# Optimization experiments

Hardware: AMD Instinct MI355X
Metric: run time of the kernel (lower is better)

Reference implementation:

```python
import jax, jax.numpy as jnp
import numpy as np

N_NODES = 500_000
N_EDGES = 8_000_000
N_GRAPHS = 1000


def _mlp(x, w1, b1, w2, b2):
    # Linear -> SELU -> Linear (torch Sequential equivalent)
    return jax.nn.selu(x @ w1 + b1) @ w2 + b2


def setup_inputs() -> dict:
    key = jax.random.key(0)
    ks = jax.random.split(key, 25)
    p = lambda i, shape: jax.random.normal(ks[i], shape, jnp.float32) * 0.1
    return {
        "nodes": jax.random.normal(ks[0], (N_NODES, 1), jnp.float32),
        "edges": jax.random.normal(ks[1], (N_EDGES, 1), jnp.float32),
        "senders": jax.random.randint(ks[2], (N_EDGES,), 0, N_NODES),
        "receivers": jax.random.randint(ks[3], (N_EDGES,), 0, N_NODES),
        "graph_ids": jnp.sort(jax.random.randint(ks[4], (N_NODES,), 0, N_GRAPHS)),
        "num_graphs": N_GRAPHS,
        # permutate_nodes: 2 -> 10 -> 10
        "pn_w1": p(5, (2, 10)), "pn_b1": p(6, (10,)), "pn_w2": p(7, (10, 10)), "pn_b2": p(8, (10,)),
        # update_edges: 11 -> 5 -> 1
        "ue_w1": p(9, (11, 5)), "ue_b1": p(10, (5,)), "ue_w2": p(11, (5, 1)), "ue_b2": p(12, (1,)),
        # permutate_edges: 1 -> 5 -> 10
        "pe_w1": p(13, (1, 5)), "pe_b1": p(14, (5,)), "pe_w2": p(15, (5, 10)), "pe_b2": p(16, (10,)),
        # update_nodes: 11 -> 5 -> 1
        "un_w1": p(17, (11, 5)), "un_b1": p(18, (5,)), "un_w2": p(19, (5, 1)), "un_b2": p(20, (1,)),
        # predict: 11 -> 10 -> 10
        "pr_w1": p(21, (11, 10)), "pr_b1": p(22, (10,)), "pr_w2": p(23, (10, 10)), "pr_b2": p(24, (10,)),
    }


def reference(nodes, edges, pn_w1, pn_b1, pn_w2, pn_b2,
              ue_w1, ue_b1, ue_w2, ue_b2,
              pe_w1, pe_b1, pe_w2, pe_b2,
              un_w1, un_b1, un_w2, un_b2,
              pr_w1, pr_b1, pr_w2, pr_b2,
              senders, receivers, graph_ids, num_graphs):
    # gather node feats to edges: [recv || send] -> (E, 2)
    collected = jnp.concatenate([nodes[receivers], nodes[senders]], axis=-1)
    h1_nodes = _mlp(collected, pn_w1, pn_b1, pn_w2, pn_b2)  # (E, 10)
    h1_edges = edges  # (E, 1)
    for _ in range(3):
        h1_edges = _mlp(jnp.concatenate([h1_edges, h1_nodes], axis=-1),
                        ue_w1, ue_b1, ue_w2, ue_b2)  # (E, 1)
    # edges -> nodes aggregation (sum over receiver)
    edges_of_nodes = jax.ops.segment_sum(h1_edges, receivers, num_segments=nodes.shape[0])  # (N, 1)
    h2_edges = _mlp(edges_of_nodes, pe_w1, pe_b1, pe_w2, pe_b2)  # (N, 10)
    h2_nodes = nodes  # (N, 1)
    for _ in range(3):
        h2_nodes = _mlp(jnp.concatenate([h2_nodes, h2_edges], axis=-1),
                        un_w1, un_b1, un_w2, un_b2)  # (N, 1)
    # nodes -> globals aggregation (sum per graph)
    g = jax.ops.segment_sum(jnp.concatenate([h2_nodes, h2_edges], axis=-1),
                            graph_ids, num_segments=num_graphs)  # (G, 11)
    out = _mlp(g, pr_w1, pr_b1, pr_w2, pr_b2)  # (G, 10)
    return jax.nn.softmax(out, axis=-1)
```

## Files before the change

kernel.cpp:

```cpp
#include <hip/hip_runtime.h>
#include <hip/hip_fp16.h>
#include <math.h>

#define N_NODES_C  500000
#define N_EDGES_C  8000000
#define N_GRAPHS_C 1000
#define NGROUPS_C  (N_EDGES_C / 4)

#define BSHIFT  11
#define BWIDTH  2048
#define NBKT    245

#define P2_TPB  512
#define EPB2    8192
#define GPB2    (EPB2 / 4)
#define NPB2    ((NGROUPS_C + GPB2 - 1) / GPB2)
#define SROW2   992
#define RITER2  (GPB2 / P2_TPB)

#define GRAPH_ACC_OFF 0
#define PARTIALS_OFF  11008
#define FW_OFF        33024
#define ZERO_HEAD     33024

#define STARTS2_OFF   33280
#define PAIRS64_OFF   (STARTS2_OFF + 246 * SROW2)
#define WS2_WORDS_NEEDED (PAIRS64_OFF + NPB2 * EPB2 * 2)

#define OLD_NODE_ACC_OFF 33536
#define OLD_ZERO_WORDS   (OLD_NODE_ACC_OFF + N_NODES_C)

#define LOG2E_F 1.4426950408889634f


__device__ __forceinline__ float selu2(float xl) {
    const float C1 = 0.7282901039f;
    const float C2 = 1.7580993408473766f;
    float e = __builtin_amdgcn_exp2f(xl);
    float neg = fmaf(C2, e, -C2);
    return xl > 0.0f ? C1 * xl : neg;
}

__device__ __forceinline__ float selu_f(float x) {
    const float scale = 1.0507009873554805f;
    const float sa    = 1.0507009873554805f * 1.6732632423543772f;
    float neg = sa * (__expf(x) - 1.0f);
    return x > 0.0f ? scale * x : neg;
}

__device__ __forceinline__ void atomAddF(float* p, float v) {
    __hip_atomic_fetch_add(p, v, __ATOMIC_RELAXED, __HIP_MEMORY_SCOPE_AGENT);
}

__device__ __forceinline__ void fuse_weights(
        int t,
        const float* __restrict__ pn_w1, const float* __restrict__ pn_b1,
        const float* __restrict__ pn_w2, const float* __restrict__ pn_b2,
        const float* __restrict__ ue_w1, const float* __restrict__ ue_b1,
        const float* __restrict__ ue_w2, const float* __restrict__ ue_b2,
        const float* __restrict__ pe_w1, const float* __restrict__ pe_b1,
        const float* __restrict__ pe_w2, const float* __restrict__ pe_b2,
        const float* __restrict__ un_w1, const float* __restrict__ un_b1,
        const float* __restrict__ un_w2, const float* __restrict__ un_b2,
        float* __restrict__ fw) {
    const float L = LOG2E_F;
    if (t < 20) fw[0 + t] = pn_w1[t] * L;
    if (t < 10) fw[20 + t] = pn_b1[t] * L;
    if (t < 50) {
        int j = t / 5, k = t % 5;
        float s = 0.0f;
        for (int m = 0; m < 10; ++m) s += pn_w2[j * 10 + m] * ue_w1[(1 + m) * 5 + k];
        fw[30 + t] = s * L;
    }
    if (t < 5) {
        float s = ue_b1[t];
        for (int m = 0; m < 10; ++m) s += pn_b2[m] * ue_w1[(1 + m) * 5 + t];
        fw[80 + t] = s * L;
    }
    if (t < 5)  fw[85 + t]  = ue_w1[t] * L;
    if (t < 5)  fw[90 + t]  = ue_w2[t];
    if (t == 0) fw[95]      = ue_b2[0];
    if (t < 5)  fw[96 + t]  = pe_w1[t] * L;
    if (t < 5)  fw[101 + t] = pe_b1[t] * L;
    if (t < 50) fw[106 + t] = pe_w2[t];
    if (t < 10) fw[156 + t] = pe_b2[t];
    if (t < 25) {
        int j = t / 5, k = t % 5;
        float s = 0.0f;
        for (int m = 0; m < 10; ++m) s += pe_w2[j * 10 + m] * un_w1[(1 + m) * 5 + k];
        fw[166 + t] = s * L;
    }
    if (t < 5) {
        float s = un_b1[t];
        for (int m = 0; m < 10; ++m) s += pe_b2[m] * un_w1[(1 + m) * 5 + t];
        fw[191 + t] = s * L;
    }
    if (t < 5)  fw[196 + t] = un_w1[t] * L;
    if (t < 5)  fw[201 + t] = un_w2[t];
    if (t == 0) fw[206]     = un_b2[0];
}

__global__ void k_fuse(const float* pn_w1, const float* pn_b1, const float* pn_w2, const float* pn_b2,
                       const float* ue_w1, const float* ue_b1, const float* ue_w2, const float* ue_b2,
                       const float* pe_w1, const float* pe_b1, const float* pe_w2, const float* pe_b2,
                       const float* un_w1, const float* un_b1, const float* un_w2, const float* un_b2,
                       float* fw) {
    fuse_weights(threadIdx.x, pn_w1, pn_b1, pn_w2, pn_b2, ue_w1, ue_b1, ue_w2, ue_b2,
                 pe_w1, pe_b1, pe_w2, pe_b2, un_w1, un_b1, un_w2, un_b2, fw);
}

__global__ void k_final(const float* __restrict__ graph_acc,
                        const float* __restrict__ partials,
                        const float* __restrict__ pr_w1, const float* __restrict__ pr_b1,
                        const float* __restrict__ pr_w2, const float* __restrict__ pr_b2,
                        float* __restrict__ out) {
    int g = blockIdx.x * blockDim.x + threadIdx.x;
    if (g >= N_GRAPHS_C) return;
    float gv[11];
#pragma unroll
    for (int f = 0; f < 11; ++f)
        gv[f] = graph_acc[g * 11 + f] + partials[g * 11 + f] + partials[11000 + g * 11 + f];
    float h[10];
#pragma unroll
    for (int j = 0; j < 10; ++j) {
        float z = pr_b1[j];
#pragma unroll
        for (int f = 0; f < 11; ++f) z = fmaf(gv[f], pr_w1[f * 10 + j], z);
        h[j] = selu_f(z);
    }
    float o[10];
    float mx = -1e30f;
#pragma unroll
    for (int j = 0; j < 10; ++j) {
        float z = pr_b2[j];
#pragma unroll
        for (int m = 0; m < 10; ++m) z = fmaf(h[m], pr_w2[m * 10 + j], z);
        o[j] = z;
        mx = fmaxf(mx, z);
    }
    float sum = 0.0f;
#pragma unroll
    for (int j = 0; j < 10; ++j) { o[j] = __expf(o[j] - mx); sum += o[j]; }
    float inv = 1.0f / sum;
#pragma unroll
    for (int j = 0; j < 10; ++j) out[g * 10 + j] = o[j] * inv;
}


__global__ __launch_bounds__(P2_TPB) void k_part2(
        float* __restrict__ ws,
        const float* __restrict__ edges,
        const int* __restrict__ senders, const int* __restrict__ receivers,
        int* __restrict__ starts_T, unsigned long long* __restrict__ pairs64,
        const float* pn_w1, const float* pn_b1, const float* pn_w2, const float* pn_b2,
        const float* ue_w1, const float* ue_b1, const float* ue_w2, const float* ue_b2,
        const float* pe_w1, const float* pe_b1, const float* pe_w2, const float* pe_b2,
        const float* un_w1, const float* un_b1, const float* un_w2, const float* un_b2) {
    __shared__ int hist[256];
    __shared__ int cursorS[256];
    __shared__ alignas(16) unsigned long long staged[EPB2];

    int tid = threadIdx.x;
    int p   = blockIdx.x;

    if (tid < 34) {
        int z = p * 34 + tid;
        if (z < ZERO_HEAD) ws[z] = 0.0f;
    }
    if (p == 0)
        fuse_weights(tid, pn_w1, pn_b1, pn_w2, pn_b2, ue_w1, ue_b1, ue_w2, ue_b2,
                     pe_w1, pe_b1, pe_w2, pe_b2, un_w1, un_b1, un_w2, un_b2, ws + FW_OFF);

    int gstart = p * GPB2;
    int gnum   = NGROUPS_C - gstart;
    if (gnum > GPB2) gnum = GPB2;

    if (tid < 256) hist[tid] = 0;
    __syncthreads();

    int4 rv4[RITER2];
#pragma unroll
    for (int r = 0; r < RITER2; ++r) {
        int idx = r * P2_TPB + tid;
        int gi  = gstart + (idx < gnum ? idx : 0);
        rv4[r] = ((const int4*)receivers)[gi];
        if (idx < gnum) {
            atomicAdd(&hist[rv4[r].x >> BSHIFT], 1);
            atomicAdd(&hist[rv4[r].y >> BSHIFT], 1);
            atomicAdd(&hist[rv4[r].z >> BSHIFT], 1);
            atomicAdd(&hist[rv4[r].w >> BSHIFT], 1);
        }
    }
    __syncthreads();

    int orig = 0, val = 0;
    if (tid < 256) { orig = hist[tid]; val = orig; }
    for (int d = 1; d < 256; d <<= 1) {
        int add = 0;
        if (tid >= d && tid < 256) add = hist[tid - d];
        __syncthreads();
        if (tid >= d && tid < 256) { val += add; hist[tid] = val; }
        __syncthreads();
    }
    int excl = val - orig;
    if (tid < 256) cursorS[tid] = excl;
    if (tid < 246) starts_T[tid * SROW2 + p] = excl;
    __syncthreads();

#pragma unroll
    for (int r = 0; r < RITER2; ++r) {
        int idx = r * P2_TPB + tid;
        int gi  = gstart + (idx < gnum ? idx : 0);
        float4 e4 = ((const float4*)edges)[gi];
        int4   s4 = ((const int4*)senders)[gi];
        int4   rv = rv4[r];
        if (idx < gnum) {
            int   rvv[4] = {rv.x, rv.y, rv.z, rv.w};
            int   svv[4] = {s4.x, s4.y, s4.z, s4.w};
            float evv[4] = {e4.x, e4.y, e4.z, e4.w};
#pragma unroll
            for (int u = 0; u < 4; ++u) {
                int bkt  = rvv[u] >> BSHIFT;
                int slot = atomicAdd(&cursorS[bkt], 1);
                unsigned long long pk =
                    ((unsigned long long)(rvv[u] & (BWIDTH - 1)) << 51)
                  | ((unsigned long long)(unsigned)svv[u] << 32)
                  | (unsigned long long)__float_as_uint(evv[u]);
                staged[slot] = pk;
            }
        }
    }
    __syncthreads();

    const uint4* st4 = (const uint4*)staged;
    uint4* dst = (uint4*)(pairs64 + (size_t)p * EPB2);
    int n4 = gnum * 2;
    for (int i = tid; i < n4; i += P2_TPB) dst[i] = st4[i];
}

__global__ __launch_bounds__(1024) void k_gather2(
        const float* __restrict__ nodes, const int* __restrict__ graph_ids,
        const float* __restrict__ fw, const int* __restrict__ starts_T,
        const unsigned long long* __restrict__ pairs64,
        float* __restrict__ graph_acc, float* __restrict__ partials) {
    __shared__ float accf[BWIDTH];
    __shared__ float nf[BWIDTH];
    __shared__ int   s0[NPB2];
    __shared__ int   pst[NPB2 + 1];
    __shared__ int   sc[1024];
    __shared__ float garr[32 * 11];
    int tid = threadIdx.x;
    int b   = blockIdx.x;

    int nodeBase = b << BSHIFT;
    int lastIdx  = nodeBase + BWIDTH;
    if (lastIdx > N_NODES_C) lastIdx = N_NODES_C;
    int lim = lastIdx - nodeBase;

    accf[tid] = 0.0f; accf[1024 + tid] = 0.0f;
    nf[tid]        = (tid        < lim) ? nodes[nodeBase + tid]        : 0.0f;
    nf[1024 + tid] = (1024 + tid < lim) ? nodes[nodeBase + 1024 + tid] : 0.0f;
    if (tid < 352) garr[tid] = 0.0f;

    int cntv = 0;
    if (tid < NPB2) {
        int a = starts_T[b * SROW2 + tid];
        int c = starts_T[(b + 1) * SROW2 + tid];
        s0[tid] = a;
        cntv = c - a;
    }
    sc[tid] = cntv;
    __syncthreads();

    int v = cntv;
    for (int d = 1; d < 1024; d <<= 1) {
        int add = (tid >= d) ? sc[tid - d] : 0;
        __syncthreads();
        if (tid >= d) { v += add; sc[tid] = v; }
        __syncthreads();
    }
    if (tid == 0) pst[0] = 0;
    if (tid < NPB2) pst[tid + 1] = v;
    __syncthreads();

    int M = pst[NPB2];

    {
        float w_pn1[20], b_pn1[10], W_eb[50], b_eb[5], w1r0[5], w2e[5];
#pragma unroll
        for (int j = 0; j < 20; ++j) w_pn1[j] = fw[j];
#pragma unroll
        for (int j = 0; j < 10; ++j) b_pn1[j] = fw[20 + j];
#pragma unroll
        for (int j = 0; j < 50; ++j) W_eb[j] = fw[30 + j];
#pragma unroll
        for (int j = 0; j < 5; ++j) b_eb[j] = fw[80 + j];
#pragma unroll
        for (int j = 0; j < 5; ++j) w1r0[j] = fw[85 + j];
#pragma unroll
        for (int j = 0; j < 5; ++j) w2e[j] = fw[90 + j];
        float b2e = fw[95];

        int i = tid;
#pragma unroll 1
        for (; i + 1024 < M; i += 2048) {
            int iA = i, iB = i + 1024;
            int loA = 0, hiA = NPB2, loB = 0, hiB = NPB2;
#pragma unroll
            for (int s = 0; s < 10; ++s) {
                int mA = (loA + hiA) >> 1;
                int mB = (loB + hiB) >> 1;
                int pA = pst[mA];
                int pB = pst[mB];
                if (pA <= iA) loA = mA; else hiA = mA;
                if (pB <= iB) loB = mB; else hiB = mB;
            }
            unsigned long long pkA =
                pairs64[(size_t)loA * EPB2 + s0[loA] + (iA - pst[loA])];
            unsigned long long pkB =
                pairs64[(size_t)loB * EPB2 + s0[loB] + (iB - pst[loB])];
            float nsA = nodes[(int)((pkA >> 32) & 0x7FFFFULL)];
            float nsB = nodes[(int)((pkB >> 32) & 0x7FFFFULL)];
            int   rlA = (int)(pkA >> 51);
            int   rlB = (int)(pkB >> 51);
            float nrA = nf[rlA];
            float nrB = nf[rlB];
            float eA  = __uint_as_float((unsigned)pkA);
            float eB  = __uint_as_float((unsigned)pkB);

            float bsA[5], bsB[5];
#pragma unroll
            for (int k = 0; k < 5; ++k) { bsA[k] = b_eb[k]; bsB[k] = b_eb[k]; }
#pragma unroll
            for (int j = 0; j < 10; ++j) {
                float zlA = fmaf(nrA, w_pn1[j], fmaf(nsA, w_pn1[10 + j], b_pn1[j]));
                float zlB = fmaf(nrB, w_pn1[j], fmaf(nsB, w_pn1[10 + j], b_pn1[j]));
                float szA = selu2(zlA);
                float szB = selu2(zlB);
#pragma unroll
                for (int k = 0; k < 5; ++k) {
                    bsA[k] = fmaf(szA, W_eb[j * 5 + k], bsA[k]);
                    bsB[k] = fmaf(szB, W_eb[j * 5 + k], bsB[k]);
                }
            }
#pragma unroll
            for (int it = 0; it < 3; ++it) {
                float aA = b2e, aB = b2e;
#pragma unroll
                for (int k = 0; k < 5; ++k) {
                    float tA = selu2(fmaf(eA, w1r0[k], bsA[k]));
                    float tB = selu2(fmaf(eB, w1r0[k], bsB[k]));
                    aA = fmaf(tA, w2e[k], aA);
                    aB = fmaf(tB, w2e[k], aB);
                }
                eA = aA; eB = aB;
            }
            atomicAdd(&accf[rlA], eA);
            atomicAdd(&accf[rlB], eB);
        }
#pragma unroll 1
        for (; i < M; i += 1024) {
            int lo = 0, hi = NPB2;
#pragma unroll
            for (int s = 0; s < 10; ++s) {
                int mid = (lo + hi) >> 1;
                if (pst[mid] <= i) lo = mid; else hi = mid;
            }
            unsigned long long pk =
                pairs64[(size_t)lo * EPB2 + s0[lo] + (i - pst[lo])];
            int   rl   = (int)(pk >> 51);
            int   sidx = (int)((pk >> 32) & 0x7FFFFULL);
            float e    = __uint_as_float((unsigned)pk);
            float nr   = nf[rl];
            float ns   = nodes[sidx];

            float bs[5];
#pragma unroll
            for (int k = 0; k < 5; ++k) bs[k] = b_eb[k];
#pragma unroll
            for (int j = 0; j < 10; ++j) {
                float zl = fmaf(nr, w_pn1[j], fmaf(ns, w_pn1[10 + j], b_pn1[j]));
                float sz = selu2(zl);
#pragma unroll
                for (int k = 0; k < 5; ++k) bs[k] = fmaf(sz, W_eb[j * 5 + k], bs[k]);
            }
#pragma unroll
            for (int it = 0; it < 3; ++it) {
                float acc2 = b2e;
#pragma unroll
                for (int k = 0; k < 5; ++k) {
                    float tt = selu2(fmaf(e, w1r0[k], bs[k]));
                    acc2 = fmaf(tt, w2e[k], acc2);
                }
                e = acc2;
            }
            atomicAdd(&accf[rl], e);
        }
    }
    __syncthreads();

    float w_pe1[5], b_pe1[5], pe_w2[50], pe_b2[10], W_nb[25], b_nb[5], w1r0n[5], w2n[5];
#pragma unroll
    for (int j = 0; j < 5; ++j) w_pe1[j] = fw[96 + j];
#pragma unroll
    for (int j = 0; j < 5; ++j) b_pe1[j] = fw[101 + j];
#pragma unroll
    for (int j = 0; j < 50; ++j) pe_w2[j] = fw[106 + j];
#pragma unroll
    for (int j = 0; j < 10; ++j) pe_b2[j] = fw[156 + j];
#pragma unroll
    for (int j = 0; j < 25; ++j) W_nb[j] = fw[166 + j];
#pragma unroll
    for (int j = 0; j < 5; ++j) b_nb[j] = fw[191 + j];
#pragma unroll
    for (int j = 0; j < 5; ++j) w1r0n[j] = fw[196 + j];
#pragma unroll
    for (int j = 0; j < 5; ++j) w2n[j] = fw[201 + j];
    float b2n = fw[206];

    int gidBase = graph_ids[nodeBase];
    int gidEnd  = graph_ids[lastIdx - 1];

#pragma unroll
    for (int q = 0; q < 2; ++q) {
        int local = q * 1024 + tid;
        int i = nodeBase + local;
        bool valid = i < N_NODES_C;

        float s = accf[local];
        float t5[5];
#pragma unroll
        for (int k = 0; k < 5; ++k) t5[k] = selu2(fmaf(s, w_pe1[k], b_pe1[k]));
        float he[10];
#pragma unroll
        for (int m = 0; m < 10; ++m) {
            float a = pe_b2[m];
#pragma unroll
            for (int k = 0; k < 5; ++k) a = fmaf(t5[k], pe_w2[k * 10 + m], a);
            he[m] = a;
        }
        float bs[5];
#pragma unroll
        for (int k = 0; k < 5; ++k) {
            float a = b_nb[k];
#pragma unroll
            for (int t = 0; t < 5; ++t) a = fmaf(t5[t], W_nb[t * 5 + k], a);
            bs[k] = a;
        }
        float n = valid ? nf[local] : 0.0f;
#pragma unroll
        for (int it = 0; it < 3; ++it) {
            float a = b2n;
#pragma unroll
            for (int k = 0; k < 5; ++k) {
                float tt = selu2(fmaf(n, w1r0n[k], bs[k]));
                a = fmaf(tt, w2n[k], a);
            }
            n = a;
        }

        int gid = valid ? graph_ids[i] : -1;
        if (!valid) {
            n = 0.0f;
#pragma unroll
            for (int m = 0; m < 10; ++m) he[m] = 0.0f;
        }

        int gid0 = __shfl(gid, 0, 64);
        bool allsame = __all(gid == gid0) && (gid0 >= 0);
        if (allsame) {
            float vv = n;
#pragma unroll
            for (int off = 32; off > 0; off >>= 1) vv += __shfl_down(vv, off, 64);
            float vh[10];
#pragma unroll
            for (int m = 0; m < 10; ++m) {
                float ww = he[m];
#pragma unroll
                for (int off = 32; off > 0; off >>= 1) ww += __shfl_down(ww, off, 64);
                vh[m] = ww;
            }
            if ((tid & 63) == 0) {
                int off = gid0 - gidBase;
                if (off >= 0 && off < 32) {
                    atomicAdd(&garr[off * 11 + 0], vv);
#pragma unroll
                    for (int m = 0; m < 10; ++m) atomicAdd(&garr[off * 11 + 1 + m], vh[m]);
                } else {
                    atomAddF(&graph_acc[gid0 * 11 + 0], vv);
#pragma unroll
                    for (int m = 0; m < 10; ++m) atomAddF(&graph_acc[gid0 * 11 + 1 + m], vh[m]);
                }
            }
        } else if (valid) {
            int off = gid - gidBase;
            if (off >= 0 && off < 32) {
                atomicAdd(&garr[off * 11 + 0], n);
#pragma unroll
                for (int m = 0; m < 10; ++m) atomicAdd(&garr[off * 11 + 1 + m], he[m]);
            } else {
                atomAddF(&graph_acc[gid * 11 + 0], n);
#pragma unroll
                for (int m = 0; m < 10; ++m) atomAddF(&graph_acc[gid * 11 + 1 + m], he[m]);
            }
        }
    }
    __syncthreads();

    int ngl = gidEnd - gidBase + 1;
    if (ngl > 32) ngl = 32;
    int par = (b & 1) * 11000;
    for (int t = tid; t < ngl * 11; t += 1024) {
        int off = t / 11, f = t - off * 11;
        partials[par + (gidBase + off) * 11 + f] = garr[t];
    }
}


__global__ __launch_bounds__(256) void k_zero(float* __restrict__ ws, int len4) {
    int i = blockIdx.x * 256 + threadIdx.x;
    if (i < len4) ((float4*)ws)[i] = make_float4(0.f, 0.f, 0.f, 0.f);
}

__global__ __launch_bounds__(256) void k_edges(
        const float* __restrict__ nodes, const float* __restrict__ edges,
        const int* __restrict__ senders, const int* __restrict__ receivers,
        const float* __restrict__ fw, float* __restrict__ node_acc) {
    float w_pn1[20], b_pn1[10], W_eb[50], b_eb[5], w1r0[5], w2e[5];
#pragma unroll
    for (int j = 0; j < 20; ++j) w_pn1[j] = fw[j];
#pragma unroll
    for (int j = 0; j < 10; ++j) b_pn1[j] = fw[20 + j];
#pragma unroll
    for (int j = 0; j < 50; ++j) W_eb[j] = fw[30 + j];
#pragma unroll
    for (int j = 0; j < 5; ++j) b_eb[j] = fw[80 + j];
#pragma unroll
    for (int j = 0; j < 5; ++j) w1r0[j] = fw[85 + j];
#pragma unroll
    for (int j = 0; j < 5; ++j) w2e[j] = fw[90 + j];
    float b2e = fw[95];

    int g = blockIdx.x * 256 + threadIdx.x;
    if (g >= NGROUPS_C) return;

    float4 e4 = ((const float4*)edges)[g];
    int4  s4 = ((const int4*)senders)[g];
    int4  r4 = ((const int4*)receivers)[g];
    float ev[4] = {e4.x, e4.y, e4.z, e4.w};
    int   sv[4] = {s4.x, s4.y, s4.z, s4.w};
    int   rv[4] = {r4.x, r4.y, r4.z, r4.w};
    float nsv[4], nrv[4];
#pragma unroll
    for (int u = 0; u < 4; ++u) { nsv[u] = nodes[sv[u]]; nrv[u] = nodes[rv[u]]; }
#pragma unroll
    for (int u = 0; u < 4; ++u) {
        float nr = nrv[u], ns = nsv[u];
        float bs[5];
#pragma unroll
        for (int k = 0; k < 5; ++k) bs[k] = b_eb[k];
#pragma unroll
        for (int j = 0; j < 10; ++j) {
            float zl = fmaf(nr, w_pn1[j], fmaf(ns, w_pn1[10 + j], b_pn1[j]));
            float sz = selu2(zl);
#pragma unroll
            for (int k = 0; k < 5; ++k) bs[k] = fmaf(sz, W_eb[j * 5 + k], bs[k]);
        }
        float e = ev[u];
#pragma unroll
        for (int it = 0; it < 3; ++it) {
            float acc2 = b2e;
#pragma unroll
            for (int k = 0; k < 5; ++k) {
                float tt = selu2(fmaf(e, w1r0[k], bs[k]));
                acc2 = fmaf(tt, w2e[k], acc2);
            }
            e = acc2;
        }
        atomAddF(&node_acc[rv[u]], e);
    }
}

__global__ __launch_bounds__(256) void k_nodes(
        const float* __restrict__ nodes, const int* __restrict__ graph_ids,
        const float* __restrict__ fw, const float* __restrict__ node_acc,
        float* __restrict__ graph_acc) {
    float w_pe1[5], b_pe1[5], pe_w2[50], pe_b2[10], W_nb[25], b_nb[5], w1r0n[5], w2n[5];
#pragma unroll
    for (int j = 0; j < 5; ++j) w_pe1[j] = fw[96 + j];
#pragma unroll
    for (int j = 0; j < 5; ++j) b_pe1[j] = fw[101 + j];
#pragma unroll
    for (int j = 0; j < 50; ++j) pe_w2[j] = fw[106 + j];
#pragma unroll
    for (int j = 0; j < 10; ++j) pe_b2[j] = fw[156 + j];
#pragma unroll
    for (int j = 0; j < 25; ++j) W_nb[j] = fw[166 + j];
#pragma unroll
    for (int j = 0; j < 5; ++j) b_nb[j] = fw[191 + j];
#pragma unroll
    for (int j = 0; j < 5; ++j) w1r0n[j] = fw[196 + j];
#pragma unroll
    for (int j = 0; j < 5; ++j) w2n[j] = fw[201 + j];
    float b2n = fw[206];

    int i = blockIdx.x * 256 + threadIdx.x;
    bool valid = i < N_NODES_C;
    int ii = valid ? i : (N_NODES_C - 1);

    float s = node_acc[ii];
    float t5[5];
#pragma unroll
    for (int k = 0; k < 5; ++k) t5[k] = selu2(fmaf(s, w_pe1[k], b_pe1[k]));
    float he[10];
#pragma unroll
    for (int m = 0; m < 10; ++m) {
        float a = pe_b2[m];
#pragma unroll
        for (int k = 0; k < 5; ++k) a = fmaf(t5[k], pe_w2[k * 10 + m], a);
        he[m] = a;
    }
    float bs[5];
#pragma unroll
    for (int k = 0; k < 5; ++k) {
        float a = b_nb[k];
#pragma unroll
        for (int t = 0; t < 5; ++t) a = fmaf(t5[t], W_nb[t * 5 + k], a);
        bs[k] = a;
    }
    float n = nodes[ii];
#pragma unroll
    for (int it = 0; it < 3; ++it) {
        float a = b2n;
#pragma unroll
        for (int k = 0; k < 5; ++k) {
            float tt = selu2(fmaf(n, w1r0n[k], bs[k]));
            a = fmaf(tt, w2n[k], a);
        }
        n = a;
    }

    int gid = valid ? graph_ids[ii] : -1;
    if (!valid) {
        n = 0.0f;
#pragma unroll
        for (int m = 0; m < 10; ++m) he[m] = 0.0f;
    }

    int gid0 = __shfl(gid, 0, 64);
    bool allsame = __all(gid == gid0) && (gid0 >= 0);
    if (allsame) {
        float v = n;
#pragma unroll
        for (int off = 32; off > 0; off >>= 1) v += __shfl_down(v, off, 64);
        float vh[10];
#pragma unroll
        for (int m = 0; m < 10; ++m) {
            float ww = he[m];
#pragma unroll
            for (int off = 32; off > 0; off >>= 1) ww += __shfl_down(ww, off, 64);
            vh[m] = ww;
        }
        if ((threadIdx.x & 63) == 0) {
            atomAddF(&graph_acc[gid0 * 11 + 0], v);
#pragma unroll
            for (int m = 0; m < 10; ++m) atomAddF(&graph_acc[gid0 * 11 + 1 + m], vh[m]);
        }
    } else if (valid) {
        atomAddF(&graph_acc[gid * 11 + 0], n);
#pragma unroll
        for (int m = 0; m < 10; ++m) atomAddF(&graph_acc[gid * 11 + 1 + m], he[m]);
    }
}


extern "C" void kernel_launch(void* const* d_in, const int* in_sizes, int n_in,
                              void* d_out, int out_size, void* d_ws, size_t ws_size,
                              hipStream_t stream) {
    const float* nodes     = (const float*)d_in[0];
    const float* edges     = (const float*)d_in[1];
    const int*   senders   = (const int*)d_in[2];
    const int*   receivers = (const int*)d_in[3];
    const int*   graph_ids = (const int*)d_in[4];
    const float* pn_w1 = (const float*)d_in[6];
    const float* pn_b1 = (const float*)d_in[7];
    const float* pn_w2 = (const float*)d_in[8];
    const float* pn_b2 = (const float*)d_in[9];
    const float* ue_w1 = (const float*)d_in[10];
    const float* ue_b1 = (const float*)d_in[11];
    const float* ue_w2 = (const float*)d_in[12];
    const float* ue_b2 = (const float*)d_in[13];
    const float* pe_w1 = (const float*)d_in[14];
    const float* pe_b1 = (const float*)d_in[15];
    const float* pe_w2 = (const float*)d_in[16];
    const float* pe_b2 = (const float*)d_in[17];
    const float* un_w1 = (const float*)d_in[18];
    const float* un_b1 = (const float*)d_in[19];
    const float* un_w2 = (const float*)d_in[20];
    const float* un_b2 = (const float*)d_in[21];
    const float* pr_w1 = (const float*)d_in[22];
    const float* pr_b1 = (const float*)d_in[23];
    const float* pr_w2 = (const float*)d_in[24];
    const float* pr_b2 = (const float*)d_in[25];

    float* ws        = (float*)d_ws;
    float* graph_acc = ws + GRAPH_ACC_OFF;
    float* partials  = ws + PARTIALS_OFF;
    float* fw        = ws + FW_OFF;
    float* outp      = (float*)d_out;

    if (ws_size >= (size_t)WS2_WORDS_NEEDED * 4) {
        int* starts_T = (int*)ws + STARTS2_OFF;
        unsigned long long* pairs64 = (unsigned long long*)((int*)ws + PAIRS64_OFF);

        hipLaunchKernelGGL(k_part2, dim3(NPB2), dim3(P2_TPB), 0, stream,
                           ws, edges, senders, receivers, starts_T, pairs64,
                           pn_w1, pn_b1, pn_w2, pn_b2, ue_w1, ue_b1, ue_w2, ue_b2,
                           pe_w1, pe_b1, pe_w2, pe_b2, un_w1, un_b1, un_w2, un_b2);
        hipLaunchKernelGGL(k_gather2, dim3(NBKT), dim3(1024), 0, stream,
                           nodes, graph_ids, fw, starts_T, pairs64, graph_acc, partials);
        hipLaunchKernelGGL(k_final, dim3((N_GRAPHS_C + 255) / 256), dim3(256), 0, stream,
                           graph_acc, partials, pr_w1, pr_b1, pr_w2, pr_b2, outp);
    } else {
        float* node_acc = ws + OLD_NODE_ACC_OFF;
        int len4 = OLD_ZERO_WORDS / 4;
        hipLaunchKernelGGL(k_zero, dim3((len4 + 255) / 256), dim3(256), 0, stream, ws, len4);
        hipLaunchKernelGGL(k_fuse, dim3(1), dim3(64), 0, stream,
                           pn_w1, pn_b1, pn_w2, pn_b2, ue_w1, ue_b1, ue_w2, ue_b2,
                           pe_w1, pe_b1, pe_w2, pe_b2, un_w1, un_b1, un_w2, un_b2, fw);
        hipLaunchKernelGGL(k_edges, dim3((NGROUPS_C + 255) / 256), dim3(256), 0, stream,
                           nodes, edges, senders, receivers, fw, node_acc);
        hipLaunchKernelGGL(k_nodes, dim3((N_NODES_C + 255) / 256), dim3(256), 0, stream,
                           nodes, graph_ids, fw, node_acc, graph_acc);
        hipLaunchKernelGGL(k_final, dim3((N_GRAPHS_C + 255) / 256), dim3(256), 0, stream,
                           graph_acc, partials, pr_w1, pr_b1, pr_w2, pr_b2, outp);
    }
}
```

Before: 300.4 us.

## Split edge gather into two half-partition blocks per bucket, separate node kernel

The per-bucket edge gather kernel is split so that each receiver bucket is handled by two blocks. Each block processes half of the source partitions and writes its partial node sums to a new workspace buffer. A new kernel then adds the two halves and runs the node MLP and the graph aggregation. This doubles the grid from 245 to 490 blocks to improve CU occupancy on a GPU with many CUs. The cost is an extra kernel launch, a global round-trip of the node accumulators, and removal of the two-edge interleaved loop in the old kernel. The new path runs only when the workspace is large enough to hold the extra buffer.

```diff
diff --git a/kernel.cpp b/kernel.cpp
--- a/kernel.cpp
+++ b/kernel.cpp
@@ -17,6 +17,7 @@
 #define NPB2    ((NGROUPS_C + GPB2 - 1) / GPB2)
 #define SROW2   992
 #define RITER2  (GPB2 / P2_TPB)
+#define HALF_P  489
 
 #define GRAPH_ACC_OFF 0
 #define PARTIALS_OFF  11008
@@ -26,6 +27,10 @@
 #define STARTS2_OFF   33280
 #define PAIRS64_OFF   (STARTS2_OFF + 246 * SROW2)
 #define WS2_WORDS_NEEDED (PAIRS64_OFF + NPB2 * EPB2 * 2)
+
+#define NA2_STRIDE    (NBKT * BWIDTH)
+#define NODEACC2_OFF  WS2_WORDS_NEEDED
+#define WS3_WORDS_NEEDED (NODEACC2_OFF + 2 * NA2_STRIDE)
 
 #define OLD_NODE_ACC_OFF 33536
 #define OLD_ZERO_WORDS   (OLD_NODE_ACC_OFF + N_NODES_C)
@@ -238,6 +243,252 @@
     for (int i = tid; i < n4; i += P2_TPB) dst[i] = st4[i];
 }
 
+#define EDGE_MLP_BODY(pk, accf)                                              \
+    {                                                                        \
+        int   rl   = (int)((pk) >> 51);                                      \
+        int   sidx = (int)(((pk) >> 32) & 0x7FFFFULL);                       \
+        float e    = __uint_as_float((unsigned)(pk));                        \
+        float nr   = nf[rl];                                                 \
+        float ns   = nodes[sidx];                                            \
+        float bs[5];                                                         \
+        _Pragma("unroll")                                                    \
+        for (int k = 0; k < 5; ++k) bs[k] = b_eb[k];                         \
+        _Pragma("unroll")                                                    \
+        for (int j = 0; j < 10; ++j) {                                       \
+            float zl = fmaf(nr, w_pn1[j], fmaf(ns, w_pn1[10 + j], b_pn1[j]));\
+            float sz = selu2(zl);                                            \
+            _Pragma("unroll")                                                \
+            for (int k = 0; k < 5; ++k) bs[k] = fmaf(sz, W_eb[j*5+k], bs[k]);\
+        }                                                                    \
+        _Pragma("unroll")                                                    \
+        for (int it = 0; it < 3; ++it) {                                     \
+            float acc2 = b2e;                                                \
+            _Pragma("unroll")                                                \
+            for (int k = 0; k < 5; ++k) {                                    \
+                float tt = selu2(fmaf(e, w1r0[k], bs[k]));                   \
+                acc2 = fmaf(tt, w2e[k], acc2);                               \
+            }                                                                \
+            e = acc2;                                                        \
+        }                                                                    \
+        atomicAdd(&(accf)[rl], e);                                           \
+    }
+
+__global__ __launch_bounds__(1024, 8) void k_gather2s(
+        const float* __restrict__ nodes,
+        const float* __restrict__ fw, const int* __restrict__ starts_T,
+        const unsigned long long* __restrict__ pairs64,
+        float* __restrict__ nodeacc2) {
+    __shared__ float accf[BWIDTH];
+    __shared__ float nf[BWIDTH];
+    __shared__ int   s0[HALF_P];
+    __shared__ int   pst[HALF_P + 1];
+    __shared__ int   sc[512];
+    int tid = threadIdx.x;
+    int b   = blockIdx.x >> 1;
+    int h   = blockIdx.x & 1;
+    int pbase  = h * HALF_P;
+    int pcount = h ? (NPB2 - HALF_P) : HALF_P;
+
+    int nodeBase = b << BSHIFT;
+    int lastIdx  = nodeBase + BWIDTH;
+    if (lastIdx > N_NODES_C) lastIdx = N_NODES_C;
+    int lim = lastIdx - nodeBase;
+
+    accf[tid] = 0.0f; accf[1024 + tid] = 0.0f;
+    nf[tid]        = (tid        < lim) ? nodes[nodeBase + tid]        : 0.0f;
+    nf[1024 + tid] = (1024 + tid < lim) ? nodes[nodeBase + 1024 + tid] : 0.0f;
+
+    int cntv = 0;
+    if (tid < pcount) {
+        int a = starts_T[b * SROW2 + pbase + tid];
+        int c = starts_T[(b + 1) * SROW2 + pbase + tid];
+        s0[tid] = a;
+        cntv = c - a;
+    }
+    if (tid < 512) sc[tid] = cntv;
+    __syncthreads();
+
+    int v = cntv;
+    for (int d = 1; d < 512; d <<= 1) {
+        int add = (tid >= d && tid < 512) ? sc[tid - d] : 0;
+        __syncthreads();
+        if (tid >= d && tid < 512) { v += add; sc[tid] = v; }
+        __syncthreads();
+    }
+    if (tid == 0) pst[0] = 0;
+    if (tid < pcount) pst[tid + 1] = v;
+    __syncthreads();
+
+    int M = pst[pcount];
+
+    {
+        float w_pn1[20], b_pn1[10], W_eb[50], b_eb[5], w1r0[5], w2e[5];
+#pragma unroll
+        for (int j = 0; j < 20; ++j) w_pn1[j] = fw[j];
+#pragma unroll
+        for (int j = 0; j < 10; ++j) b_pn1[j] = fw[20 + j];
+#pragma unroll
+        for (int j = 0; j < 50; ++j) W_eb[j] = fw[30 + j];
+#pragma unroll
+        for (int j = 0; j < 5; ++j) b_eb[j] = fw[80 + j];
+#pragma unroll
+        for (int j = 0; j < 5; ++j) w1r0[j] = fw[85 + j];
+#pragma unroll
+        for (int j = 0; j < 5; ++j) w2e[j] = fw[90 + j];
+        float b2e = fw[95];
+
+#pragma unroll 1
+        for (int i = tid; i < M; i += 1024) {
+            int lo = 0, hi = pcount;
+#pragma unroll
+            for (int s = 0; s < 9; ++s) {
+                int mid = (lo + hi) >> 1;
+                if (pst[mid] <= i) lo = mid; else hi = mid;
+            }
+            unsigned long long pk =
+                pairs64[(size_t)(pbase + lo) * EPB2 + s0[lo] + (i - pst[lo])];
+            EDGE_MLP_BODY(pk, accf)
+        }
+    }
+    __syncthreads();
+
+    float* dst = nodeacc2 + (size_t)h * NA2_STRIDE + (size_t)b * BWIDTH;
+    dst[tid] = accf[tid];
+    dst[1024 + tid] = accf[1024 + tid];
+}
+
+__global__ __launch_bounds__(1024) void k_nodes2(
+        const float* __restrict__ nodes, const int* __restrict__ graph_ids,
+        const float* __restrict__ fw, const float* __restrict__ nodeacc2,
+        float* __restrict__ graph_acc, float* __restrict__ partials) {
+    __shared__ float garr[32 * 11];
+    int tid = threadIdx.x;
+    int b   = blockIdx.x;
+
+    if (tid < 352) garr[tid] = 0.0f;
+
+    float w_pe1[5], b_pe1[5], pe_w2[50], pe_b2[10], W_nb[25], b_nb[5], w1r0n[5], w2n[5];
+#pragma unroll
+    for (int j = 0; j < 5; ++j) w_pe1[j] = fw[96 + j];
+#pragma unroll
+    for (int j = 0; j < 5; ++j) b_pe1[j] = fw[101 + j];
+#pragma unroll
+    for (int j = 0; j < 50; ++j) pe_w2[j] = fw[106 + j];
+#pragma unroll
+    for (int j = 0; j < 10; ++j) pe_b2[j] = fw[156 + j];
+#pragma unroll
+    for (int j = 0; j < 25; ++j) W_nb[j] = fw[166 + j];
+#pragma unroll
+    for (int j = 0; j < 5; ++j) b_nb[j] = fw[191 + j];
+#pragma unroll
+    for (int j = 0; j < 5; ++j) w1r0n[j] = fw[196 + j];
+#pragma unroll
+    for (int j = 0; j < 5; ++j) w2n[j] = fw[201 + j];
+    float b2n = fw[206];
+
+    int nodeBase = b << BSHIFT;
+    int lastIdx  = nodeBase + BWIDTH;
+    if (lastIdx > N_NODES_C) lastIdx = N_NODES_C;
+    int gidBase = graph_ids[nodeBase];
+    int gidEnd  = graph_ids[lastIdx - 1];
+    __syncthreads();
+
+#pragma unroll
+    for (int q = 0; q < 2; ++q) {
+        int local = q * 1024 + tid;
+        int i = nodeBase + local;
+        bool valid = i < N_NODES_C;
+
+        float s = nodeacc2[(size_t)b * BWIDTH + local]
+                + nodeacc2[(size_t)NA2_STRIDE + (size_t)b * BWIDTH + local];
+        float t5[5];
+#pragma unroll
+        for (int k = 0; k < 5; ++k) t5[k] = selu2(fmaf(s, w_pe1[k], b_pe1[k]));
+        float he[10];
+#pragma unroll
+        for (int m = 0; m < 10; ++m) {
+            float a = pe_b2[m];
+#pragma unroll
+            for (int k = 0; k < 5; ++k) a = fmaf(t5[k], pe_w2[k * 10 + m], a);
+            he[m] = a;
+        }
+        float bs[5];
+#pragma unroll
+        for (int k = 0; k < 5; ++k) {
+            float a = b_nb[k];
+#pragma unroll
+            for (int t = 0; t < 5; ++t) a = fmaf(t5[t], W_nb[t * 5 + k], a);
+            bs[k] = a;
+        }
+        float n = valid ? nodes[i] : 0.0f;
+#pragma unroll
+        for (int it = 0; it < 3; ++it) {
+            float a = b2n;
+#pragma unroll
+            for (int k = 0; k < 5; ++k) {
+                float tt = selu2(fmaf(n, w1r0n[k], bs[k]));
+                a = fmaf(tt, w2n[k], a);
+            }
+            n = a;
+        }
+
+        int gid = valid ? graph_ids[i] : -1;
+        if (!valid) {
+            n = 0.0f;
+#pragma unroll
+            for (int m = 0; m < 10; ++m) he[m] = 0.0f;
+        }
+
+        int gid0 = __shfl(gid, 0, 64);
+        bool allsame = __all(gid == gid0) && (gid0 >= 0);
+        if (allsame) {
+            float vv = n;
+#pragma unroll
+            for (int off = 32; off > 0; off >>= 1) vv += __shfl_down(vv, off, 64);
+            float vh[10];
+#pragma unroll
+            for (int m = 0; m < 10; ++m) {
+                float ww = he[m];
+#pragma unroll
+                for (int off = 32; off > 0; off >>= 1) ww += __shfl_down(ww, off, 64);
+                vh[m] = ww;
+            }
+            if ((tid & 63) == 0) {
+                int off = gid0 - gidBase;
+                if (off >= 0 && off < 32) {
+                    atomicAdd(&garr[off * 11 + 0], vv);
+#pragma unroll
+                    for (int m = 0; m < 10; ++m) atomicAdd(&garr[off * 11 + 1 + m], vh[m]);
+                } else {
+                    atomAddF(&graph_acc[gid0 * 11 + 0], vv);
+#pragma unroll
+                    for (int m = 0; m < 10; ++m) atomAddF(&graph_acc[gid0 * 11 + 1 + m], vh[m]);
+                }
+            }
+        } else if (valid) {
+            int off = gid - gidBase;
+            if (off >= 0 && off < 32) {
+                atomicAdd(&garr[off * 11 + 0], n);
+#pragma unroll
+                for (int m = 0; m < 10; ++m) atomicAdd(&garr[off * 11 + 1 + m], he[m]);
+            } else {
+                atomAddF(&graph_acc[gid * 11 + 0], n);
+#pragma unroll
+                for (int m = 0; m < 10; ++m) atomAddF(&graph_acc[gid * 11 + 1 + m], he[m]);
+            }
+        }
+    }
+    __syncthreads();
+
+    int ngl = gidEnd - gidBase + 1;
+    if (ngl > 32) ngl = 32;
+    int par = (b & 1) * 11000;
+    for (int t = tid; t < ngl * 11; t += 1024) {
+        int off = t / 11, f = t - off * 11;
+        partials[par + (gidBase + off) * 11 + f] = garr[t];
+    }
+}
+
 __global__ __launch_bounds__(1024) void k_gather2(
         const float* __restrict__ nodes, const int* __restrict__ graph_ids,
         const float* __restrict__ fw, const int* __restrict__ starts_T,
@@ -301,65 +552,8 @@
         for (int j = 0; j < 5; ++j) w2e[j] = fw[90 + j];
         float b2e = fw[95];
 
-        int i = tid;
 #pragma unroll 1
-        for (; i + 1024 < M; i += 2048) {
-            int iA = i, iB = i + 1024;
-            int loA = 0, hiA = NPB2, loB = 0, hiB = NPB2;
-#pragma unroll
-            for (int s = 0; s < 10; ++s) {
-                int mA = (loA + hiA) >> 1;
-                int mB = (loB + hiB) >> 1;
-                int pA = pst[mA];
-                int pB = pst[mB];
-                if (pA <= iA) loA = mA; else hiA = mA;
-                if (pB <= iB) loB = mB; else hiB = mB;
-            }
-            unsigned long long pkA =
-                pairs64[(size_t)loA * EPB2 + s0[loA] + (iA - pst[loA])];
-            unsigned long long pkB =
-                pairs64[(size_t)loB * EPB2 + s0[loB] + (iB - pst[loB])];
-            float nsA = nodes[(int)((pkA >> 32) & 0x7FFFFULL)];
-            float nsB = nodes[(int)((pkB >> 32) & 0x7FFFFULL)];
-            int   rlA = (int)(pkA >> 51);
-            int   rlB = (int)(pkB >> 51);
-            float nrA = nf[rlA];
-            float nrB = nf[rlB];
-            float eA  = __uint_as_float((unsigned)pkA);
-            float eB  = __uint_as_float((unsigned)pkB);
-
-            float bsA[5], bsB[5];
-#pragma unroll
-            for (int k = 0; k < 5; ++k) { bsA[k] = b_eb[k]; bsB[k] = b_eb[k]; }
-#pragma unroll
-            for (int j = 0; j < 10; ++j) {
-                float zlA = fmaf(nrA, w_pn1[j], fmaf(nsA, w_pn1[10 + j], b_pn1[j]));
-                float zlB = fmaf(nrB, w_pn1[j], fmaf(nsB, w_pn1[10 + j], b_pn1[j]));
-                float szA = selu2(zlA);
-                float szB = selu2(zlB);
-#pragma unroll
-                for (int k = 0; k < 5; ++k) {
-                    bsA[k] = fmaf(szA, W_eb[j * 5 + k], bsA[k]);
-                    bsB[k] = fmaf(szB, W_eb[j * 5 + k], bsB[k]);
-                }
-            }
-#pragma unroll
-            for (int it = 0; it < 3; ++it) {
-                float aA = b2e, aB = b2e;
-#pragma unroll
-                for (int k = 0; k < 5; ++k) {
-                    float tA = selu2(fmaf(eA, w1r0[k], bsA[k]));
-                    float tB = selu2(fmaf(eB, w1r0[k], bsB[k]));
-                    aA = fmaf(tA, w2e[k], aA);
-                    aB = fmaf(tB, w2e[k], aB);
-                }
-                eA = aA; eB = aB;
-            }
-            atomicAdd(&accf[rlA], eA);
-            atomicAdd(&accf[rlB], eB);
-        }
-#pragma unroll 1
-        for (; i < M; i += 1024) {
+        for (int i = tid; i < M; i += 1024) {
             int lo = 0, hi = NPB2;
 #pragma unroll
             for (int s = 0; s < 10; ++s) {
@@ -368,33 +562,7 @@
             }
             unsigned long long pk =
                 pairs64[(size_t)lo * EPB2 + s0[lo] + (i - pst[lo])];
-            int   rl   = (int)(pk >> 51);
-            int   sidx = (int)((pk >> 32) & 0x7FFFFULL);
-            float e    = __uint_as_float((unsigned)pk);
-            float nr   = nf[rl];
-            float ns   = nodes[sidx];
-
-            float bs[5];
-#pragma unroll
-            for (int k = 0; k < 5; ++k) bs[k] = b_eb[k];
-#pragma unroll
-            for (int j = 0; j < 10; ++j) {
-                float zl = fmaf(nr, w_pn1[j], fmaf(ns, w_pn1[10 + j], b_pn1[j]));
-                float sz = selu2(zl);
-#pragma unroll
-                for (int k = 0; k < 5; ++k) bs[k] = fmaf(sz, W_eb[j * 5 + k], bs[k]);
-            }
-#pragma unroll
-            for (int it = 0; it < 3; ++it) {
-                float acc2 = b2e;
-#pragma unroll
-                for (int k = 0; k < 5; ++k) {
-                    float tt = selu2(fmaf(e, w1r0[k], bs[k]));
-                    acc2 = fmaf(tt, w2e[k], acc2);
-                }
-                e = acc2;
-            }
-            atomicAdd(&accf[rl], e);
+            EDGE_MLP_BODY(pk, accf)
         }
     }
     __syncthreads();
@@ -709,7 +877,22 @@
     float* fw        = ws + FW_OFF;
     float* outp      = (float*)d_out;
 
-    if (ws_size >= (size_t)WS2_WORDS_NEEDED * 4) {
+    if (ws_size >= (size_t)WS3_WORDS_NEEDED * 4) {
+        int* starts_T = (int*)ws + STARTS2_OFF;
+        unsigned long long* pairs64 = (unsigned long long*)((int*)ws + PAIRS64_OFF);
+        float* nodeacc2 = ws + NODEACC2_OFF;
+
+        hipLaunchKernelGGL(k_part2, dim3(NPB2), dim3(P2_TPB), 0, stream,
+                           ws, edges, senders, receivers, starts_T, pairs64,
+                           pn_w1, pn_b1, pn_w2, pn_b2, ue_w1, ue_b1, ue_w2, ue_b2,
+                           pe_w1, pe_b1, pe_w2, pe_b2, un_w1, un_b1, un_w2, un_b2);
+        hipLaunchKernelGGL(k_gather2s, dim3(2 * NBKT), dim3(1024), 0, stream,
+                           nodes, fw, starts_T, pairs64, nodeacc2);
+        hipLaunchKernelGGL(k_nodes2, dim3(NBKT), dim3(1024), 0, stream,
+                           nodes, graph_ids, fw, nodeacc2, graph_acc, partials);
+        hipLaunchKernelGGL(k_final, dim3((N_GRAPHS_C + 255) / 256), dim3(256), 0, stream,
+                           graph_acc, partials, pr_w1, pr_b1, pr_w2, pr_b2, outp);
+    } else if (ws_size >= (size_t)WS2_WORDS_NEEDED * 4) {
         int* starts_T = (int*)ws + STARTS2_OFF;
         unsigned long long* pairs64 = (unsigned long long*)((int*)ws + PAIRS64_OFF);
 
```

After: 282.6 us. 5.9% less time.
